# Kernel optimization log

Hardware: AMD Instinct MI355X
Metric: run time of the kernel (lower is better)

The kernel has to match this reference:

```python
import jax, jax.numpy as jnp
import numpy as np

DIM = 4096
N_HEADS = 32
N_KV = 8
HEAD_DIM = DIM // N_HEADS  # 128
R = N_HEADS // N_KV        # 4 query heads per kv head
B, T = 2, 2048


def setup_inputs() -> dict:
    key = jax.random.key(0)
    kx, kq, kkv, ko = jax.random.split(key, 4)
    scale = 0.02
    return {
        "x": jax.random.normal(kx, (B, T, DIM), dtype=jnp.float32),
        "Wq": jax.random.normal(kq, (DIM, DIM), dtype=jnp.float32) * scale,
        "Wkv": jax.random.normal(kkv, (2 * N_KV * HEAD_DIM, DIM), dtype=jnp.float32) * scale,
        "Wo": jax.random.normal(ko, (DIM, DIM), dtype=jnp.float32) * scale,
    }


def reference(x, Wq, Wkv, Wo):
    Bs, Ts, C = x.shape
    # projections (torch Linear: y = x @ W.T)
    q = (x @ Wq.T).reshape(Bs, Ts, N_HEADS, HEAD_DIM).transpose(0, 2, 1, 3)  # [B,H,T,hd]
    kv = x @ Wkv.T                                                            # [B,T,2*KV*hd]
    k, v = jnp.split(kv, 2, axis=-1)
    k = k.reshape(Bs, Ts, N_KV, HEAD_DIM).transpose(0, 2, 1, 3)  # [B,KV,T,hd]
    v = v.reshape(Bs, Ts, N_KV, HEAD_DIM).transpose(0, 2, 1, 3)  # [B,KV,T,hd]
    # grouped query heads: head h = g*R + r matches repeat_interleave(R, dim=1)
    qg = q.reshape(Bs, N_KV, R, Ts, HEAD_DIM)                    # [B,KV,R,T,hd]
    inv_scale = 1.0 / np.sqrt(HEAD_DIM).astype(np.float32)
    scores = jnp.einsum("bgrtd,bgsd->bgrts", qg, k) * inv_scale  # [B,KV,R,T,T]
    causal = jnp.tril(jnp.ones((Ts, Ts), dtype=bool))
    scores = jnp.where(causal, scores, jnp.finfo(scores.dtype).min)
    attn = jax.nn.softmax(scores, axis=-1)
    o = jnp.einsum("bgrts,bgsd->bgrtd", attn, v)                 # [B,KV,R,T,hd]
    o = o.reshape(Bs, N_HEADS, Ts, HEAD_DIM).transpose(0, 2, 1, 3).reshape(Bs, Ts, C)
    return o @ Wo.T
```

## Files before the change

kernel.cpp:

```cpp
#include <hip/hip_runtime.h>
#include <hip/hip_bf16.h>
#include <cstdint>
#include <type_traits>

#define DIM    4096
#define NHEADS 32
#define NKVH   8
#define HD     128
#define BATCH  2
#define SEQ    2048
#define MROWS  (BATCH*SEQ)
#define NQKV   6144
#define KOFF   4096
#define VOFF   5120

typedef __attribute__((ext_vector_type(8))) __bf16 bf16x8;
typedef __attribute__((ext_vector_type(4))) __bf16 bf16x4;
typedef __attribute__((ext_vector_type(4))) float  f32x4;

#define QSCALE 0.1275174338f

__device__ __forceinline__ void gl_lds16(const __bf16* g, __bf16* l) {
    __builtin_amdgcn_global_load_lds(
        (const __attribute__((address_space(1))) void*)g,
        (__attribute__((address_space(3))) void*)l, 16, 0, 0);
}

__global__ void cast_f32_bf16(const float* __restrict__ s, __bf16* __restrict__ d, int n8) {
    int i = blockIdx.x * 256 + threadIdx.x;
    if (i >= n8) return;
    float4 a = ((const float4*)s)[2*i];
    float4 b = ((const float4*)s)[2*i+1];
    bf16x8 v;
    v[0]=(__bf16)a.x; v[1]=(__bf16)a.y; v[2]=(__bf16)a.z; v[3]=(__bf16)a.w;
    v[4]=(__bf16)b.x; v[5]=(__bf16)b.y; v[6]=(__bf16)b.z; v[7]=(__bf16)b.w;
    ((bf16x8*)d)[i] = v;
}

template<typename OutT>
__global__ __launch_bounds__(256)
void gemm_bt(const __bf16* __restrict__ A, const __bf16* __restrict__ Bm,
             OutT* __restrict__ C, int M, int N, int K,
             float scale, int scale_cols)
{
    __shared__ __bf16 As[128*64];
    __shared__ __bf16 Bs[128*64];
    const int tid  = threadIdx.x;
    const int lane = tid & 63;
    const int w    = tid >> 6;
    const int quad = lane >> 4;
    const int l16  = lane & 15;
    const int m0   = blockIdx.y * 128;
    const int n0   = blockIdx.x * 128;
    const int wm   = (w & 1) * 64;
    const int wn   = (w >> 1) * 64;

    const __bf16* Ab = A  + (size_t)m0 * K;
    const __bf16* Bb = Bm + (size_t)n0 * K;

    f32x4 acc[4][4] = {};

    for (int k0 = 0; k0 < K; k0 += 64) {
        __syncthreads();
        #pragma unroll
        for (int r = 0; r < 4; ++r) {
            int chunk = r*256 + tid;
            int row = chunk >> 3, c8 = chunk & 7;
            int c8s = c8 ^ (row & 7);
            gl_lds16(Ab + (size_t)row*K + k0 + c8s*8, As + chunk*8);
            gl_lds16(Bb + (size_t)row*K + k0 + c8s*8, Bs + chunk*8);
        }
        __syncthreads();
        #pragma unroll
        for (int t = 0; t < 2; ++t) {
            bf16x8 af[4], bfr[4];
            #pragma unroll
            for (int i = 0; i < 4; ++i) {
                int row = wm + i*16 + l16;
                int cc  = (t*4 + quad) ^ (row & 7);
                af[i] = *(const bf16x8*)(As + row*64 + cc*8);
            }
            #pragma unroll
            for (int j = 0; j < 4; ++j) {
                int row = wn + j*16 + l16;
                int cc  = (t*4 + quad) ^ (row & 7);
                bfr[j] = *(const bf16x8*)(Bs + row*64 + cc*8);
            }
            #pragma unroll
            for (int i = 0; i < 4; ++i)
                #pragma unroll
                for (int j = 0; j < 4; ++j)
                    acc[i][j] = __builtin_amdgcn_mfma_f32_16x16x32_bf16(af[i], bfr[j], acc[i][j], 0,0,0);
        }
    }

    #pragma unroll
    for (int i = 0; i < 4; ++i) {
        #pragma unroll
        for (int j = 0; j < 4; ++j) {
            int col = n0 + wn + j*16 + l16;
            float sc = (col < scale_cols) ? scale : 1.0f;
            #pragma unroll
            for (int r = 0; r < 4; ++r) {
                int row = m0 + wm + i*16 + quad*4 + r;
                float v = acc[i][j][r] * sc;
                if constexpr (std::is_same<OutT, float>::value)
                    C[(size_t)row * N + col] = v;
                else
                    C[(size_t)row * N + col] = (__bf16)v;
            }
        }
    }
}

__global__ void transpose_v(const __bf16* __restrict__ qkv, __bf16* __restrict__ vt) {
    int idx  = blockIdx.x * 256 + threadIdx.x;
    int s8   = idx & 255;
    int rest = idx >> 8;
    int d    = rest & (HD-1);
    int bg   = rest >> 7;
    int b    = bg >> 3;
    int g    = bg & 7;
    int s0   = s8 * 8;
    const __bf16* src = qkv + (size_t)(b*SEQ + s0)*NQKV + VOFF + g*HD + d;
    bf16x8 v;
    #pragma unroll
    for (int u = 0; u < 8; ++u) v[u] = src[(size_t)u*NQKV];
    *(bf16x8*)(vt + (size_t)rest*SEQ + s0) = v;
}

__global__ __launch_bounds__(512, 4)
void flash_attn(const __bf16* __restrict__ qkv, const __bf16* __restrict__ vt,
                __bf16* __restrict__ O)
{
    __shared__ __bf16 Ks[2][64*128];
    __shared__ __bf16 Vts[2][128*64];
    __shared__ __bf16 Ps[128*64];

    const int qt = (gridDim.x - 1) - blockIdx.x;
    const int bh = blockIdx.y;
    const int b  = bh >> 5;
    const int h  = bh & 31;
    const int g  = h >> 2;
    const int q0 = qt * 128;

    const int tid  = threadIdx.x;
    const int lane = tid & 63;
    const int w    = tid >> 6;
    const int quad = lane >> 4;
    const int l16  = lane & 15;
    const int psw  = (l16 & 7) << 1;

    const __bf16* Qb  = qkv + (size_t)(b*SEQ + q0)*NQKV + h*HD;
    const __bf16* Kb  = qkv + (size_t)(b*SEQ)*NQKV + KOFF + g*HD;
    const __bf16* Vtb = vt  + (size_t)((b*NKVH + g)*HD)*SEQ;

    bf16x8 qf[4];
    #pragma unroll
    for (int t = 0; t < 4; ++t)
        qf[t] = *(const bf16x8*)(Qb + (size_t)(w*16 + l16)*NQKV + t*32 + quad*8);

    f32x4 o_acc[8] = {};
    float m_i = -1e30f, l_i = 0.f;
    const int myrow = q0 + w*16 + l16;
    const int wmin  = q0 + w*16;

    const int nkt = 2*qt + 2;

    #pragma unroll
    for (int r = 0; r < 2; ++r) {
        int c = r*512 + tid;
        { int row = c >> 4, c16 = c & 15;
          int c16s = c16 ^ (row & 7);
          gl_lds16(Kb + (size_t)row*NQKV + c16s*8, &Ks[0][0] + c*8); }
        { int dd = c >> 3, c8 = c & 7;
          int c8s = c8 ^ (dd & 7);
          gl_lds16(Vtb + (size_t)dd*SEQ + c8s*8, &Vts[0][0] + c*8); }
    }
    __syncthreads();

    int cur = 0;
    for (int kt = 0; kt < nkt; ++kt) {
        const int s0 = kt * 64;

        if (kt + 1 < nkt) {
            const int sn = s0 + 64;
            __bf16* Ksb  = &Ks[cur^1][0];
            __bf16* Vtsb = &Vts[cur^1][0];
            #pragma unroll
            for (int r = 0; r < 2; ++r) {
                int c = r*512 + tid;
                { int row = c >> 4, c16 = c & 15;
                  int c16s = c16 ^ (row & 7);
                  gl_lds16(Kb + (size_t)(sn + row)*NQKV + c16s*8, Ksb + c*8); }
                { int dd = c >> 3, c8 = c & 7;
                  int c8s = c8 ^ (dd & 7);
                  gl_lds16(Vtb + (size_t)dd*SEQ + sn + c8s*8, Vtsb + c*8); }
            }
        }

        if (s0 <= wmin + 15) {
            const __bf16* Ksb  = &Ks[cur][0];
            const __bf16* Vtsb = &Vts[cur][0];

            f32x4 s_acc[4] = {};
            #pragma unroll
            for (int t = 0; t < 4; ++t) {
                #pragma unroll
                for (int j = 0; j < 4; ++j) {
                    int row = j*16 + l16;
                    int cc  = (t*4 + quad) ^ (row & 7);
                    bf16x8 bk = *(const bf16x8*)(Ksb + row*128 + cc*8);
                    s_acc[j] = __builtin_amdgcn_mfma_f32_16x16x32_bf16(bk, qf[t], s_acc[j], 0,0,0);
                }
            }

            if (s0 + 63 > wmin) {
                #pragma unroll
                for (int j = 0; j < 4; ++j)
                    #pragma unroll
                    for (int r = 0; r < 4; ++r)
                        if (s0 + j*16 + quad*4 + r > myrow) s_acc[j][r] = -1e30f;
            }

            float pm = s_acc[0][0];
            #pragma unroll
            for (int j = 0; j < 4; ++j)
                #pragma unroll
                for (int r = 0; r < 4; ++r)
                    pm = fmaxf(pm, s_acc[j][r]);
            pm = fmaxf(pm, __shfl_xor(pm, 16));
            pm = fmaxf(pm, __shfl_xor(pm, 32));
            float mnew  = fmaxf(m_i, pm);
            float alpha = exp2f(m_i - mnew);
            m_i = mnew;

            float psum = 0.f;
            #pragma unroll
            for (int j = 0; j < 4; ++j) {
                bf16x4 pv;
                #pragma unroll
                for (int r = 0; r < 4; ++r) {
                    float p = exp2f(s_acc[j][r] - mnew);
                    psum += p;
                    pv[r] = (__bf16)p;
                }
                int cs = (j*4 + quad) ^ psw;
                *(bf16x4*)(Ps + (w*16 + l16)*64 + cs*4) = pv;
            }
            psum += __shfl_xor(psum, 16);
            psum += __shfl_xor(psum, 32);
            l_i = l_i*alpha + psum;

            float av[4];
            #pragma unroll
            for (int r = 0; r < 4; ++r) av[r] = __shfl(alpha, quad*4 + r);
            #pragma unroll
            for (int jt = 0; jt < 8; ++jt)
                #pragma unroll
                for (int r = 0; r < 4; ++r)
                    o_acc[jt][r] *= av[r];

            #pragma unroll
            for (int t = 0; t < 2; ++t) {
                int cs = (t*8 + quad*2) ^ psw;
                bf16x8 ap = *(const bf16x8*)(Ps + (w*16 + l16)*64 + cs*4);
                #pragma unroll
                for (int jt = 0; jt < 8; ++jt) {
                    int row = jt*16 + l16;
                    int cc  = (t*4 + quad) ^ (row & 7);
                    bf16x8 bv = *(const bf16x8*)(Vtsb + row*64 + cc*8);
                    o_acc[jt] = __builtin_amdgcn_mfma_f32_16x16x32_bf16(ap, bv, o_acc[jt], 0,0,0);
                }
            }
        }

        __syncthreads();
        cur ^= 1;
    }

    float inv = 1.0f / l_i;
    float ivr[4];
    #pragma unroll
    for (int r = 0; r < 4; ++r) ivr[r] = __shfl(inv, quad*4 + r);
    #pragma unroll
    for (int jt = 0; jt < 8; ++jt) {
        #pragma unroll
        for (int r = 0; r < 4; ++r) {
            int row = q0 + w*16 + quad*4 + r;
            int col = h*HD + jt*16 + l16;
            O[(size_t)(b*SEQ + row)*DIM + col] = (__bf16)(o_acc[jt][r] * ivr[r]);
        }
    }
}

extern "C" void kernel_launch(void* const* d_in, const int* in_sizes, int n_in,
                              void* d_out, int out_size, void* d_ws, size_t ws_size,
                              hipStream_t stream) {
    const float* x   = (const float*)d_in[0];
    const float* Wq  = (const float*)d_in[1];
    const float* Wkv = (const float*)d_in[2];
    const float* Wo  = (const float*)d_in[3];

    const size_t OFF_XB   = 0;
    const size_t OFF_WQKV = 33554432;
    const size_t OFF_WO   = 83886080;
    const size_t OFF_QKV  = 117440512;
    const size_t OFF_VT   = 167772160;
    const size_t OFF_OB   = 176160768;
    const size_t NEEDED   = 209715200;
    if (ws_size < NEEDED) return;

    char* ws = (char*)d_ws;
    __bf16* xb   = (__bf16*)(ws + OFF_XB);
    __bf16* wqkv = (__bf16*)(ws + OFF_WQKV);
    __bf16* wo   = (__bf16*)(ws + OFF_WO);
    __bf16* qkv  = (__bf16*)(ws + OFF_QKV);
    __bf16* vt   = (__bf16*)(ws + OFF_VT);
    __bf16* ob   = (__bf16*)(ws + OFF_OB);

    cast_f32_bf16<<<16777216/8/256, 256, 0, stream>>>(x,   xb,              16777216/8);
    cast_f32_bf16<<<16777216/8/256, 256, 0, stream>>>(Wq,  wqkv,            16777216/8);
    cast_f32_bf16<<< 8388608/8/256, 256, 0, stream>>>(Wkv, wqkv + 16777216,  8388608/8);
    cast_f32_bf16<<<16777216/8/256, 256, 0, stream>>>(Wo,  wo,              16777216/8);

    gemm_bt<__bf16><<<dim3(NQKV/128, MROWS/128), 256, 0, stream>>>(
        xb, wqkv, qkv, MROWS, NQKV, DIM, QSCALE, DIM);

    transpose_v<<<524288/256, 256, 0, stream>>>(qkv, vt);

    flash_attn<<<dim3(SEQ/128, BATCH*NHEADS), 512, 0, stream>>>(qkv, vt, ob);

    gemm_bt<float><<<dim3(DIM/128, MROWS/128), 256, 0, stream>>>(
        ob, wo, (float*)d_out, MROWS, DIM, DIM, 1.0f, 0);
}
```

Before: 817.2 us.

## Use 256x256 double-buffered GEMM tiles with interleaved loads and XCD-aware block swizzle

Replaces the 128x128 single-buffered bf16 GEMM with a 256x256-tile kernel. It uses 512 threads and double-buffered LDS, and issues the next K-slab's global→LDS loads between MFMA phases so memory and compute overlap. Block indices are remapped round-robin across XCDs and MFMA phases are wrapped in s_setprio. The goal is more operand reuse per LDS load and more latency hiding. The cost is 128KB of LDS per block, which limits occupancy to one block per CU, plus extra barriers per K step.

```diff
diff --git a/kernel.cpp b/kernel.cpp
--- a/kernel.cpp
+++ b/kernel.cpp
@@ -38,64 +38,153 @@
 }
 
 template<typename OutT>
-__global__ __launch_bounds__(256)
-void gemm_bt(const __bf16* __restrict__ A, const __bf16* __restrict__ Bm,
-             OutT* __restrict__ C, int M, int N, int K,
-             float scale, int scale_cols)
+__global__ __launch_bounds__(512, 2)
+void gemm_bt256(const __bf16* __restrict__ A, const __bf16* __restrict__ Bm,
+                OutT* __restrict__ C, int M, int N, int K,
+                float scale, int scale_cols)
 {
-    __shared__ __bf16 As[128*64];
-    __shared__ __bf16 Bs[128*64];
+    __shared__ __bf16 As[2][256*64];
+    __shared__ __bf16 Bs[2][256*64];
+
+    const int nbx  = gridDim.x;
+    const int nwg  = nbx * gridDim.y;
+    const int orig = blockIdx.y * nbx + blockIdx.x;
+    const int swz  = (orig & 7) * (nwg >> 3) + (orig >> 3);
+    const int m0   = (swz / nbx) * 256;
+    const int n0   = (swz % nbx) * 256;
+
     const int tid  = threadIdx.x;
     const int lane = tid & 63;
     const int w    = tid >> 6;
     const int quad = lane >> 4;
     const int l16  = lane & 15;
-    const int m0   = blockIdx.y * 128;
-    const int n0   = blockIdx.x * 128;
-    const int wm   = (w & 1) * 64;
-    const int wn   = (w >> 1) * 64;
+    const int wm   = (w >> 2) * 128;
+    const int wn   = (w & 3)  * 64;
 
     const __bf16* Ab = A  + (size_t)m0 * K;
     const __bf16* Bb = Bm + (size_t)n0 * K;
 
-    f32x4 acc[4][4] = {};
-
-    for (int k0 = 0; k0 < K; k0 += 64) {
-        __syncthreads();
-        #pragma unroll
-        for (int r = 0; r < 4; ++r) {
-            int chunk = r*256 + tid;
+    f32x4 acc[8][4] = {};
+
+    auto stageA = [&](int buf, int k0) {
+        #pragma unroll
+        for (int i = 0; i < 4; ++i) {
+            int chunk = i*512 + tid;
             int row = chunk >> 3, c8 = chunk & 7;
             int c8s = c8 ^ (row & 7);
-            gl_lds16(Ab + (size_t)row*K + k0 + c8s*8, As + chunk*8);
-            gl_lds16(Bb + (size_t)row*K + k0 + c8s*8, Bs + chunk*8);
-        }
-        __syncthreads();
-        #pragma unroll
-        for (int t = 0; t < 2; ++t) {
-            bf16x8 af[4], bfr[4];
-            #pragma unroll
-            for (int i = 0; i < 4; ++i) {
+            gl_lds16(Ab + (size_t)row*K + k0 + c8s*8, &As[buf][0] + chunk*8);
+        }
+    };
+    auto stageB = [&](int buf, int k0) {
+        #pragma unroll
+        for (int i = 0; i < 4; ++i) {
+            int chunk = i*512 + tid;
+            int row = chunk >> 3, c8 = chunk & 7;
+            int c8s = c8 ^ (row & 7);
+            gl_lds16(Bb + (size_t)row*K + k0 + c8s*8, &Bs[buf][0] + chunk*8);
+        }
+    };
+
+    stageA(0, 0); stageB(0, 0);
+    asm volatile("s_waitcnt vmcnt(0)" ::: "memory");
+    __builtin_amdgcn_s_barrier();
+    __builtin_amdgcn_sched_barrier(0);
+
+    const int NT = K >> 6;
+    int cur = 0;
+    for (int kt = 0; kt < NT; ++kt) {
+        const int kn = (kt + 1) << 6;
+        const __bf16* Ac = &As[cur][0];
+        const __bf16* Bc = &Bs[cur][0];
+        bf16x8 af[4][2], bfr[4][2];
+
+        #pragma unroll
+        for (int i = 0; i < 4; ++i)
+            #pragma unroll
+            for (int t = 0; t < 2; ++t) {
                 int row = wm + i*16 + l16;
                 int cc  = (t*4 + quad) ^ (row & 7);
-                af[i] = *(const bf16x8*)(As + row*64 + cc*8);
-            }
-            #pragma unroll
-            for (int j = 0; j < 4; ++j) {
+                af[i][t] = *(const bf16x8*)(Ac + row*64 + cc*8);
+            }
+        #pragma unroll
+        for (int j = 0; j < 2; ++j)
+            #pragma unroll
+            for (int t = 0; t < 2; ++t) {
                 int row = wn + j*16 + l16;
                 int cc  = (t*4 + quad) ^ (row & 7);
-                bfr[j] = *(const bf16x8*)(Bs + row*64 + cc*8);
-            }
+                bfr[j][t] = *(const bf16x8*)(Bc + row*64 + cc*8);
+            }
+        if (kt + 1 < NT) stageA(cur ^ 1, kn);
+        __builtin_amdgcn_s_barrier();
+        __builtin_amdgcn_s_setprio(1);
+        #pragma unroll
+        for (int t = 0; t < 2; ++t)
             #pragma unroll
             for (int i = 0; i < 4; ++i)
                 #pragma unroll
-                for (int j = 0; j < 4; ++j)
-                    acc[i][j] = __builtin_amdgcn_mfma_f32_16x16x32_bf16(af[i], bfr[j], acc[i][j], 0,0,0);
-        }
+                for (int j = 0; j < 2; ++j)
+                    acc[i][j] = __builtin_amdgcn_mfma_f32_16x16x32_bf16(af[i][t], bfr[j][t], acc[i][j], 0,0,0);
+        __builtin_amdgcn_s_setprio(0);
+        __builtin_amdgcn_s_barrier();
+
+        #pragma unroll
+        for (int j = 2; j < 4; ++j)
+            #pragma unroll
+            for (int t = 0; t < 2; ++t) {
+                int row = wn + j*16 + l16;
+                int cc  = (t*4 + quad) ^ (row & 7);
+                bfr[j][t] = *(const bf16x8*)(Bc + row*64 + cc*8);
+            }
+        if (kt + 1 < NT) stageB(cur ^ 1, kn);
+        __builtin_amdgcn_s_barrier();
+        __builtin_amdgcn_s_setprio(1);
+        #pragma unroll
+        for (int t = 0; t < 2; ++t)
+            #pragma unroll
+            for (int i = 0; i < 4; ++i)
+                #pragma unroll
+                for (int j = 2; j < 4; ++j)
+                    acc[i][j] = __builtin_amdgcn_mfma_f32_16x16x32_bf16(af[i][t], bfr[j][t], acc[i][j], 0,0,0);
+        __builtin_amdgcn_s_setprio(0);
+        __builtin_amdgcn_s_barrier();
+
+        #pragma unroll
+        for (int i = 0; i < 4; ++i)
+            #pragma unroll
+            for (int t = 0; t < 2; ++t) {
+                int row = wm + (4 + i)*16 + l16;
+                int cc  = (t*4 + quad) ^ (row & 7);
+                af[i][t] = *(const bf16x8*)(Ac + row*64 + cc*8);
+            }
+        __builtin_amdgcn_s_barrier();
+        __builtin_amdgcn_s_setprio(1);
+        #pragma unroll
+        for (int t = 0; t < 2; ++t)
+            #pragma unroll
+            for (int i = 0; i < 4; ++i)
+                #pragma unroll
+                for (int j = 0; j < 2; ++j)
+                    acc[4 + i][j] = __builtin_amdgcn_mfma_f32_16x16x32_bf16(af[i][t], bfr[j][t], acc[4 + i][j], 0,0,0);
+        __builtin_amdgcn_s_setprio(0);
+        __builtin_amdgcn_s_barrier();
+
+        __builtin_amdgcn_s_setprio(1);
+        #pragma unroll
+        for (int t = 0; t < 2; ++t)
+            #pragma unroll
+            for (int i = 0; i < 4; ++i)
+                #pragma unroll
+                for (int j = 2; j < 4; ++j)
+                    acc[4 + i][j] = __builtin_amdgcn_mfma_f32_16x16x32_bf16(af[i][t], bfr[j][t], acc[4 + i][j], 0,0,0);
+        __builtin_amdgcn_s_setprio(0);
+        asm volatile("s_waitcnt vmcnt(0)" ::: "memory");
+        __builtin_amdgcn_s_barrier();
+        __builtin_amdgcn_sched_barrier(0);
+        cur ^= 1;
     }
 
     #pragma unroll
-    for (int i = 0; i < 4; ++i) {
+    for (int i = 0; i < 8; ++i) {
         #pragma unroll
         for (int j = 0; j < 4; ++j) {
             int col = n0 + wn + j*16 + l16;
@@ -324,13 +413,13 @@
     cast_f32_bf16<<< 8388608/8/256, 256, 0, stream>>>(Wkv, wqkv + 16777216,  8388608/8);
     cast_f32_bf16<<<16777216/8/256, 256, 0, stream>>>(Wo,  wo,              16777216/8);
 
-    gemm_bt<__bf16><<<dim3(NQKV/128, MROWS/128), 256, 0, stream>>>(
+    gemm_bt256<__bf16><<<dim3(NQKV/256, MROWS/256), 512, 0, stream>>>(
         xb, wqkv, qkv, MROWS, NQKV, DIM, QSCALE, DIM);
 
     transpose_v<<<524288/256, 256, 0, stream>>>(qkv, vt);
 
     flash_attn<<<dim3(SEQ/128, BATCH*NHEADS), 512, 0, stream>>>(qkv, vt, ob);
 
-    gemm_bt<float><<<dim3(DIM/128, MROWS/128), 256, 0, stream>>>(
+    gemm_bt256<float><<<dim3(DIM/256, MROWS/256), 512, 0, stream>>>(
         ob, wo, (float*)d_out, MROWS, DIM, DIM, 1.0f, 0);
 }
```

Result: no change. 809.7 us (-0.9%).
